# Kernel tuning notes

Measured on AMD Instinct MI355X. Metric: run time of the kernel, lower is better.

## Reference

```python
import jax, jax.numpy as jnp
import numpy as np

NUM_HEAD = 8
A_DIM = 256
M_DIM = 256
OUT_DIM = 256
KEY_DIM = A_DIM // NUM_HEAD   # 32
VALUE_DIM = M_DIM // NUM_HEAD # 32
B, NQ, NK = 128, 384, 384


def setup_inputs() -> dict:
    key = jax.random.key(0)
    ks = jax.random.split(key, 11)
    s = 0.05
    return {
        "q_data": jax.random.normal(ks[0], (B, NQ, A_DIM), jnp.float32),
        "m_data": jax.random.normal(ks[1], (B, NK, M_DIM), jnp.float32),
        "bias": jax.random.normal(ks[2], (B, NQ, NK), jnp.float32),
        "nonbatched_bias": jax.random.normal(ks[3], (NQ, NK), jnp.float32),
        "query_w": jax.random.normal(ks[4], (A_DIM, NUM_HEAD, KEY_DIM), jnp.float32) * s,
        "key_w": jax.random.normal(ks[5], (M_DIM, NUM_HEAD, KEY_DIM), jnp.float32) * s,
        "value_w": jax.random.normal(ks[6], (M_DIM, NUM_HEAD, VALUE_DIM), jnp.float32) * s,
        "gating_w": jax.random.normal(ks[7], (A_DIM, NUM_HEAD, VALUE_DIM), jnp.float32) * s,
        "gating_b": jax.random.normal(ks[8], (NUM_HEAD, VALUE_DIM), jnp.float32) * s,
        "output_w": jax.random.normal(ks[9], (NUM_HEAD, VALUE_DIM, OUT_DIM), jnp.float32) * s,
        "output_b": jax.random.normal(ks[10], (OUT_DIM,), jnp.float32) * s,
    }


def reference(q_data, m_data, bias, nonbatched_bias, query_w, key_w, value_w,
              gating_w, gating_b, output_w, output_b):
    # q: [b, q, h, c] scaled by 1/sqrt(key_dim)
    scale = KEY_DIM ** -0.5
    q = jnp.einsum('bqa,ahc->bqhc', q_data, query_w) * scale
    k = jnp.einsum('bka,ahc->bkhc', m_data, key_w)
    v = jnp.einsum('bka,ahc->bkhc', m_data, value_w)
    # logits [b, h, q, k] with per-batch bias and shared nonbatched bias
    logits = jnp.einsum('bqhc,bkhc->bhqk', q, k)
    logits = logits + bias[:, None, :, :] + nonbatched_bias[None, None, :, :]
    weights = jax.nn.softmax(logits, axis=-1)
    weighted_avg = jnp.einsum('bhqk,bkhc->bqhc', weights, v)
    # sigmoid gating
    gate = jax.nn.sigmoid(jnp.einsum('bqa,ahc->bqhc', q_data, gating_w)
                          + gating_b[None, None, :, :])
    weighted_avg = weighted_avg * gate
    # output projection
    out = jnp.einsum('bqhc,hco->bqo', weighted_avg, output_w) + output_b
    return out
```

## Files before the change

kernel.cpp:

```cpp
#include <hip/hip_runtime.h>

typedef unsigned short u16;
typedef unsigned int u32;
typedef __attribute__((ext_vector_type(8))) short bf16x8;
typedef __attribute__((ext_vector_type(4))) float f32x4;

#define BATCH 128
#define NQL   384
#define NKL   384
#define NHEAD 8
#define HD    32
#define ADIM  256
#define QSCALE 0.17677669529663689f

__device__ __forceinline__ u16 f2bf(float f) {
    union { float f; u32 u; } v; v.f = f;
    u32 r = v.u + 0x7fffu + ((v.u >> 16) & 1u);
    return (u16)(r >> 16);
}
__device__ __forceinline__ float bf2f(u16 u) {
    union { u32 u; float f; } v; v.u = ((u32)u) << 16;
    return v.f;
}
__device__ __forceinline__ u32 pk(float a, float b) {
    return (u32)f2bf(a) | ((u32)f2bf(b) << 16);
}

__global__ __launch_bounds__(256) void prep_w_kernel(
    const float* __restrict__ qw, const float* __restrict__ kw,
    const float* __restrict__ vw, const float* __restrict__ gw,
    const float* __restrict__ ow, u16* __restrict__ wt)
{
    const float* src;
    switch (blockIdx.y) {
        case 0: src = qw; break;
        case 1: src = kw; break;
        case 2: src = vw; break;
        case 3: src = gw; break;
        default: src = ow; break;
    }
    u16* dst = wt + (size_t)blockIdx.y * 65536;
    int t = threadIdx.x;
    int n0 = blockIdx.x * 16;
    for (int i = 0; i < 16; i++) {
        int n = n0 + i;
        dst[n * 256 + t] = f2bf(src[t * 256 + n]);
    }
}

__global__ __launch_bounds__(256) void proj2_kernel(
    const float* __restrict__ qd, const float* __restrict__ md,
    const u16* __restrict__ wt, const float* __restrict__ gb,
    u16* __restrict__ q_o, u16* __restrict__ k_o,
    u16* __restrict__ v_o, u16* __restrict__ g_o)
{
    const int z = blockIdx.z;
    const float* A = (z == 0) ? qd : md;
    const u16* W0 = wt + (size_t)(z == 0 ? 0 : 1) * 65536;
    const u16* W1 = wt + (size_t)(z == 0 ? 3 : 2) * 65536;
    u16* O0 = (z == 0) ? q_o : k_o;
    u16* O1 = (z == 0) ? g_o : v_o;

    const int bm = blockIdx.x * 128, bn = blockIdx.y * 128;
    const int tid = threadIdx.x;
    const int lane = tid & 63, wave = tid >> 6;
    const int col = lane & 15, quad = lane >> 4;
    const int mw = (wave & 1) * 64, nw = (wave >> 1) * 64;

    __shared__ u16 As[128][32];
    __shared__ u16 Ws0[128][32];
    __shared__ u16 Ws1[128][32];

    f32x4 acc0[4][4], acc1[4][4];
#pragma unroll
    for (int i = 0; i < 4; i++)
#pragma unroll
        for (int j = 0; j < 4; j++) {
            acc0[i][j] = (f32x4){0.f, 0.f, 0.f, 0.f};
            acc1[i][j] = (f32x4){0.f, 0.f, 0.f, 0.f};
        }

    const int arow = tid >> 1, acb = (tid & 1) * 16;
    const float* asrc = A + (size_t)(bm + arow) * 256 + acb;
    const u16*   ws0  = W0 + (size_t)(bn + arow) * 256 + acb;
    const u16*   ws1  = W1 + (size_t)(bn + arow) * 256 + acb;

    for (int k0 = 0; k0 < 256; k0 += 32) {
        __syncthreads();
        {
            float4 f0 = *(const float4*)(asrc + k0 + 0);
            float4 f1 = *(const float4*)(asrc + k0 + 4);
            float4 f2 = *(const float4*)(asrc + k0 + 8);
            float4 f3 = *(const float4*)(asrc + k0 + 12);
            uint4 u0 = make_uint4(pk(f0.x, f0.y), pk(f0.z, f0.w), pk(f1.x, f1.y), pk(f1.z, f1.w));
            uint4 u1 = make_uint4(pk(f2.x, f2.y), pk(f2.z, f2.w), pk(f3.x, f3.y), pk(f3.z, f3.w));
            *(uint4*)&As[arow][acb + 0] = u0;
            *(uint4*)&As[arow][acb + 8] = u1;
            *(uint4*)&Ws0[arow][acb + 0] = *(const uint4*)(ws0 + k0 + 0);
            *(uint4*)&Ws0[arow][acb + 8] = *(const uint4*)(ws0 + k0 + 8);
            *(uint4*)&Ws1[arow][acb + 0] = *(const uint4*)(ws1 + k0 + 0);
            *(uint4*)&Ws1[arow][acb + 8] = *(const uint4*)(ws1 + k0 + 8);
        }
        __syncthreads();
        bf16x8 bv0[4], bv1[4];
#pragma unroll
        for (int nt = 0; nt < 4; nt++) {
            bv0[nt] = *(const bf16x8*)&Ws0[nw + nt * 16 + col][quad * 8];
            bv1[nt] = *(const bf16x8*)&Ws1[nw + nt * 16 + col][quad * 8];
        }
#pragma unroll
        for (int mt = 0; mt < 4; mt++) {
            bf16x8 av = *(const bf16x8*)&As[mw + mt * 16 + col][quad * 8];
#pragma unroll
            for (int nt = 0; nt < 4; nt++) {
                acc0[mt][nt] = __builtin_amdgcn_mfma_f32_16x16x32_bf16(av, bv0[nt], acc0[mt][nt], 0, 0, 0);
                acc1[mt][nt] = __builtin_amdgcn_mfma_f32_16x16x32_bf16(av, bv1[nt], acc1[mt][nt], 0, 0, 0);
            }
        }
    }

#pragma unroll
    for (int nt = 0; nt < 4; nt++) {
        int gn = bn + nw + nt * 16 + col;
        float gbv = (z == 0) ? gb[gn] : 0.f;
#pragma unroll
        for (int mt = 0; mt < 4; mt++) {
#pragma unroll
            for (int r = 0; r < 4; r++) {
                int gm = bm + mw + mt * 16 + quad * 4 + r;
                float v0 = acc0[mt][nt][r];
                float v1 = acc1[mt][nt][r];
                if (z == 0) {
                    v0 *= QSCALE;
                    v1 = 1.f / (1.f + __expf(-(v1 + gbv)));
                }
                O0[(size_t)gm * 256 + gn] = f2bf(v0);
                O1[(size_t)gm * 256 + gn] = f2bf(v1);
            }
        }
    }
}

__global__ __launch_bounds__(256) void attn_kernel(
    const u16* __restrict__ q_ws, const u16* __restrict__ k_ws,
    const u16* __restrict__ v_ws, const u16* __restrict__ g_ws,
    const float* __restrict__ bias, const float* __restrict__ nb,
    u16* __restrict__ wa_ws)
{
    const int bi = blockIdx.x >> 3, h = blockIdx.x & 7;
    const int tid = threadIdx.x;
    const int lane = tid & 63, wave = tid >> 6;
    const int col = lane & 15, quad = lane >> 4;

    __shared__ u16 Ks[384][32];
    __shared__ u16 Vt[32 * 384];
    __shared__ __align__(16) char scratch[4][4096];
    float* Bs = (float*)scratch[wave];
    u16*   Ps = (u16*)scratch[wave];

    const u16* kg = k_ws + (size_t)bi * 384 * 256 + h * 32;
    const u16* vg = v_ws + (size_t)bi * 384 * 256 + h * 32;
    for (int f = tid * 8; f < 384 * 32; f += 256 * 8) {
        int kr = f >> 5, c = f & 31;
        *(uint4*)&Ks[kr][c] = *(const uint4*)&kg[kr * 256 + c];
    }
    for (int f = tid * 8; f < 384 * 32; f += 256 * 8) {
        int kv = f >> 5, c0 = f & 31;
        u16 tmp[8];
        *(uint4*)tmp = *(const uint4*)&vg[kv * 256 + c0];
        int kvg = kv >> 3, kvr = kv & 7;
#pragma unroll
        for (int j = 0; j < 8; j++) {
            int c = c0 + j;
            Vt[c * 384 + ((kvg ^ (c & 7)) << 3) + kvr] = tmp[j];
        }
    }
    __syncthreads();

    for (int qt = wave; qt < 24; qt += 4) {
        const int q0 = qt * 16;
        bf16x8 qf = *(const bf16x8*)(q_ws + ((size_t)(bi * 384 + q0 + col)) * 256 + h * 32 + quad * 8);

        const float* brow = bias + ((size_t)bi * 384 + q0) * 384;
        const float* nrow = nb + (size_t)q0 * 384;

        float S[24][4];
#pragma unroll
        for (int g = 0; g < 6; g++) {
#pragma unroll
            for (int i = 0; i < 4; i++) {
                int flat = lane + 64 * i;
                int row = flat >> 4, c4 = (flat & 15) << 2;
                float4 bv = *(const float4*)&brow[(size_t)row * 384 + g * 64 + c4];
                float4 nv = *(const float4*)&nrow[(size_t)row * 384 + g * 64 + c4];
                float4 sv = make_float4(bv.x + nv.x, bv.y + nv.y, bv.z + nv.z, bv.w + nv.w);
                *(float4*)&Bs[row * 64 + c4] = sv;
            }
            asm volatile("s_waitcnt lgkmcnt(0)" ::: "memory");
#pragma unroll
            for (int tt = 0; tt < 4; tt++) {
                int t = g * 4 + tt;
                f32x4 ci;
#pragma unroll
                for (int r = 0; r < 4; r++)
                    ci[r] = Bs[(quad * 4 + r) * 64 + tt * 16 + col];
                bf16x8 kf = *(const bf16x8*)&Ks[t * 16 + col][quad * 8];
                f32x4 a = __builtin_amdgcn_mfma_f32_16x16x32_bf16(qf, kf, ci, 0, 0, 0);
                S[t][0] = a[0]; S[t][1] = a[1]; S[t][2] = a[2]; S[t][3] = a[3];
            }
            asm volatile("s_waitcnt lgkmcnt(0)" ::: "memory");
        }

#pragma unroll
        for (int r = 0; r < 4; r++) {
            float m = S[0][r];
#pragma unroll
            for (int t = 1; t < 24; t++) m = fmaxf(m, S[t][r]);
#pragma unroll
            for (int o = 1; o < 16; o <<= 1) m = fmaxf(m, __shfl_xor(m, o));
            float s = 0.f;
#pragma unroll
            for (int t = 0; t < 24; t++) { float p = __expf(S[t][r] - m); S[t][r] = p; s += p; }
#pragma unroll
            for (int o = 1; o < 16; o <<= 1) s += __shfl_xor(s, o);
            float inv = 1.f / s;
#pragma unroll
            for (int t = 0; t < 24; t++) S[t][r] *= inv;
        }

        f32x4 o0 = (f32x4){0.f, 0.f, 0.f, 0.f};
        f32x4 o1 = (f32x4){0.f, 0.f, 0.f, 0.f};
#pragma unroll
        for (int g = 0; g < 6; g++) {
#pragma unroll
            for (int tt = 0; tt < 4; tt++) {
                int t = g * 4 + tt;
#pragma unroll
                for (int r = 0; r < 4; r++)
                    Ps[(quad * 4 + r) * 72 + tt * 16 + col] = f2bf(S[t][r]);
            }
            asm volatile("s_waitcnt lgkmcnt(0)" ::: "memory");
            bf16x8 a0 = *(const bf16x8*)&Ps[col * 72 + quad * 8];
            bf16x8 a1 = *(const bf16x8*)&Ps[col * 72 + 32 + quad * 8];
            const int e = col & 7;
            const int gg0 = g * 8 + quad;
            const int gg1 = gg0 + 4;
            bf16x8 b00 = *(const bf16x8*)&Vt[col * 384 + ((gg0 ^ e) << 3)];
            bf16x8 b01 = *(const bf16x8*)&Vt[col * 384 + ((gg1 ^ e) << 3)];
            bf16x8 b10 = *(const bf16x8*)&Vt[(col + 16) * 384 + ((gg0 ^ e) << 3)];
            bf16x8 b11 = *(const bf16x8*)&Vt[(col + 16) * 384 + ((gg1 ^ e) << 3)];
            o0 = __builtin_amdgcn_mfma_f32_16x16x32_bf16(a0, b00, o0, 0, 0, 0);
            o0 = __builtin_amdgcn_mfma_f32_16x16x32_bf16(a1, b01, o0, 0, 0, 0);
            o1 = __builtin_amdgcn_mfma_f32_16x16x32_bf16(a0, b10, o1, 0, 0, 0);
            o1 = __builtin_amdgcn_mfma_f32_16x16x32_bf16(a1, b11, o1, 0, 0, 0);
            asm volatile("s_waitcnt lgkmcnt(0)" ::: "memory");
        }

        const size_t rowbase = (size_t)bi * 384 + q0 + quad * 4;
#pragma unroll
        for (int r = 0; r < 4; r++) {
            size_t base = (rowbase + r) * 256 + h * 32;
            {
                size_t idx = base + col;
                wa_ws[idx] = f2bf(o0[r] * bf2f(g_ws[idx]));
            }
            {
                size_t idx = base + 16 + col;
                wa_ws[idx] = f2bf(o1[r] * bf2f(g_ws[idx]));
            }
        }
    }
}

__global__ __launch_bounds__(256) void outproj_kernel(
    const u16* __restrict__ wa, const u16* __restrict__ W,
    const float* __restrict__ ob, float* __restrict__ out)
{
    const int bm = blockIdx.x * 128, bn = blockIdx.y * 128;
    const int tid = threadIdx.x;
    const int lane = tid & 63, wave = tid >> 6;
    const int col = lane & 15, quad = lane >> 4;
    const int mw = (wave & 1) * 64, nw = (wave >> 1) * 64;

    __shared__ u16 As[128][32];
    __shared__ u16 Ws[128][32];

    f32x4 acc[4][4];
#pragma unroll
    for (int i = 0; i < 4; i++)
#pragma unroll
        for (int j = 0; j < 4; j++) acc[i][j] = (f32x4){0.f, 0.f, 0.f, 0.f};

    const int arow = tid >> 1, acb = (tid & 1) * 16;
    const u16* asrc = wa + (size_t)(bm + arow) * 256 + acb;
    const u16* wsrc = W + (size_t)(bn + arow) * 256 + acb;

    for (int k0 = 0; k0 < 256; k0 += 32) {
        __syncthreads();
        *(uint4*)&As[arow][acb + 0] = *(const uint4*)(asrc + k0 + 0);
        *(uint4*)&As[arow][acb + 8] = *(const uint4*)(asrc + k0 + 8);
        *(uint4*)&Ws[arow][acb + 0] = *(const uint4*)(wsrc + k0 + 0);
        *(uint4*)&Ws[arow][acb + 8] = *(const uint4*)(wsrc + k0 + 8);
        __syncthreads();
        bf16x8 bv[4];
#pragma unroll
        for (int nt = 0; nt < 4; nt++)
            bv[nt] = *(const bf16x8*)&Ws[nw + nt * 16 + col][quad * 8];
#pragma unroll
        for (int mt = 0; mt < 4; mt++) {
            bf16x8 av = *(const bf16x8*)&As[mw + mt * 16 + col][quad * 8];
#pragma unroll
            for (int nt = 0; nt < 4; nt++)
                acc[mt][nt] = __builtin_amdgcn_mfma_f32_16x16x32_bf16(av, bv[nt], acc[mt][nt], 0, 0, 0);
        }
    }

#pragma unroll
    for (int nt = 0; nt < 4; nt++) {
        int gn = bn + nw + nt * 16 + col;
        float obv = ob[gn];
#pragma unroll
        for (int mt = 0; mt < 4; mt++) {
#pragma unroll
            for (int r = 0; r < 4; r++) {
                int gm = bm + mw + mt * 16 + quad * 4 + r;
                out[(size_t)gm * 256 + gn] = acc[mt][nt][r] + obv;
            }
        }
    }
}

extern "C" void kernel_launch(void* const* d_in, const int* in_sizes, int n_in,
                              void* d_out, int out_size, void* d_ws, size_t ws_size,
                              hipStream_t stream)
{
    const float* q_data = (const float*)d_in[0];
    const float* m_data = (const float*)d_in[1];
    const float* bias   = (const float*)d_in[2];
    const float* nb     = (const float*)d_in[3];
    const float* qw     = (const float*)d_in[4];
    const float* kw     = (const float*)d_in[5];
    const float* vw     = (const float*)d_in[6];
    const float* gw     = (const float*)d_in[7];
    const float* gb     = (const float*)d_in[8];
    const float* ow     = (const float*)d_in[9];
    const float* ob     = (const float*)d_in[10];
    float* out = (float*)d_out;

    char* ws = (char*)d_ws;
    u16* wt = (u16*)ws;
    const size_t PROJ = (size_t)BATCH * NQL * 256;
    u16* q_ws  = (u16*)(ws + (1 << 20));
    u16* k_ws  = q_ws + PROJ;
    u16* v_ws  = k_ws + PROJ;
    u16* g_ws  = v_ws + PROJ;
    u16* wa_ws = g_ws + PROJ;

    prep_w_kernel<<<dim3(16, 5), 256, 0, stream>>>(qw, kw, vw, gw, ow, wt);
    proj2_kernel<<<dim3(384, 2, 2), 256, 0, stream>>>(q_data, m_data, wt, gb,
                                                      q_ws, k_ws, v_ws, g_ws);
    attn_kernel<<<dim3(1024), 256, 0, stream>>>(q_ws, k_ws, v_ws, g_ws,
                                                bias, nb, wa_ws);
    outproj_kernel<<<dim3(384, 2), 256, 0, stream>>>(wa_ws, wt + 4 * 65536, ob, out);
}
```

Before: 445.5 us.

## Pre-swizzle combined bias to bf16 fragments and widen projection GEMM tiles with async LDS loads

A new prep kernel sums the batched and non-batched bias once and stores it as bf16 in MFMA accumulator-fragment order. The attention kernel then loads each bias fragment directly as the MFMA C input, instead of every head re-reading and adding two fp32 bias tensors through LDS. The projection and output GEMMs move to one 256-wide N tile per block, with weight (and activation) tiles loaded into LDS through global_load_lds, and launch bounds set to allow two blocks per CU. The attention output buffer now reuses the q buffer, and block order is changed to head-major. Storing the bias in bf16 reduces precision, and the head-major ordering may reduce L2 reuse of K/V and bias across heads.

```diff
diff --git a/kernel.cpp b/kernel.cpp
--- a/kernel.cpp
+++ b/kernel.cpp
@@ -2,6 +2,7 @@
 
 typedef unsigned short u16;
 typedef unsigned int u32;
+typedef unsigned long long u64;
 typedef __attribute__((ext_vector_type(8))) short bf16x8;
 typedef __attribute__((ext_vector_type(4))) float f32x4;
 
@@ -25,6 +26,12 @@
 __device__ __forceinline__ u32 pk(float a, float b) {
     return (u32)f2bf(a) | ((u32)f2bf(b) << 16);
 }
+__device__ __forceinline__ void async_cp16(const void* g, void* l) {
+    __builtin_amdgcn_global_load_lds(
+        (const __attribute__((address_space(1))) u32*)g,
+        (__attribute__((address_space(3))) u32*)(u32)(u64)l,
+        16, 0, 0);
+}
 
 __global__ __launch_bounds__(256) void prep_w_kernel(
     const float* __restrict__ qw, const float* __restrict__ kw,
@@ -48,45 +55,70 @@
     }
 }
 
-__global__ __launch_bounds__(256) void proj2_kernel(
+__global__ __launch_bounds__(256) void prep_bias_kernel(
+    const float* __restrict__ bias, const float* __restrict__ nb,
+    u16* __restrict__ bias_sw)
+{
+    const int qt = blockIdx.x, b = blockIdx.y;
+    const int t = threadIdx.x;
+    const int lane = t & 63, sub = t >> 6;
+    const int col = lane & 15, quad = lane >> 4;
+    const float* bb = bias + ((size_t)b * 384 + qt * 16) * 384;
+    const float* nn = nb + (size_t)qt * 16 * 384;
+    u16* outb = bias_sw + ((size_t)b * 24 + qt) * 24 * 256;
+#pragma unroll
+    for (int i = 0; i < 6; i++) {
+        int kt = sub + i * 4;
+        int c = kt * 16 + col;
+        u16 v[4];
+#pragma unroll
+        for (int r = 0; r < 4; r++) {
+            int q = quad * 4 + r;
+            v[r] = f2bf(bb[(size_t)q * 384 + c] + nn[(size_t)q * 384 + c]);
+        }
+        *(uint2*)&outb[(size_t)kt * 256 + lane * 4] = *(uint2*)v;
+    }
+}
+
+__global__ __launch_bounds__(256, 2) void proj_kernel(
     const float* __restrict__ qd, const float* __restrict__ md,
     const u16* __restrict__ wt, const float* __restrict__ gb,
     u16* __restrict__ q_o, u16* __restrict__ k_o,
     u16* __restrict__ v_o, u16* __restrict__ g_o)
 {
-    const int z = blockIdx.z;
-    const float* A = (z == 0) ? qd : md;
-    const u16* W0 = wt + (size_t)(z == 0 ? 0 : 1) * 65536;
-    const u16* W1 = wt + (size_t)(z == 0 ? 3 : 2) * 65536;
-    u16* O0 = (z == 0) ? q_o : k_o;
-    u16* O1 = (z == 0) ? g_o : v_o;
-
-    const int bm = blockIdx.x * 128, bn = blockIdx.y * 128;
+    const int widx = blockIdx.x;
+    const int bm = blockIdx.y * 128;
+    const int side = blockIdx.z;
+    const float* A = side ? md : qd;
+    const int wsel = side ? (widx ? 2 : 1) : (widx ? 3 : 0);
+    const u16* W = wt + (size_t)wsel * 65536;
+    u16* O = side ? (widx ? v_o : k_o) : (widx ? g_o : q_o);
+    const int mode = side ? 0 : (widx ? 2 : 1);
+
     const int tid = threadIdx.x;
     const int lane = tid & 63, wave = tid >> 6;
     const int col = lane & 15, quad = lane >> 4;
-    const int mw = (wave & 1) * 64, nw = (wave >> 1) * 64;
-
-    __shared__ u16 As[128][32];
-    __shared__ u16 Ws0[128][32];
-    __shared__ u16 Ws1[128][32];
-
-    f32x4 acc0[4][4], acc1[4][4];
+    const int mw = (wave & 1) * 64, nsl = (wave >> 1) * 128;
+
+    __shared__ u16 Abf[128][32];
+    __shared__ u16 Wb[256][32];
+
+    f32x4 acc[4][8];
 #pragma unroll
     for (int i = 0; i < 4; i++)
 #pragma unroll
-        for (int j = 0; j < 4; j++) {
-            acc0[i][j] = (f32x4){0.f, 0.f, 0.f, 0.f};
-            acc1[i][j] = (f32x4){0.f, 0.f, 0.f, 0.f};
-        }
+        for (int j = 0; j < 8; j++) acc[i][j] = (f32x4){0.f, 0.f, 0.f, 0.f};
 
     const int arow = tid >> 1, acb = (tid & 1) * 16;
     const float* asrc = A + (size_t)(bm + arow) * 256 + acb;
-    const u16*   ws0  = W0 + (size_t)(bn + arow) * 256 + acb;
-    const u16*   ws1  = W1 + (size_t)(bn + arow) * 256 + acb;
+    const int wrow = tid >> 2, wcb = (tid & 3) * 8;
 
     for (int k0 = 0; k0 < 256; k0 += 32) {
         __syncthreads();
+#pragma unroll
+        for (int i = 0; i < 4; i++)
+            async_cp16(W + (size_t)(i * 64 + wrow) * 256 + k0 + wcb,
+                       (char*)Wb + i * 4096 + tid * 16);
         {
             float4 f0 = *(const float4*)(asrc + k0 + 0);
             float4 f1 = *(const float4*)(asrc + k0 + 4);
@@ -94,48 +126,39 @@
             float4 f3 = *(const float4*)(asrc + k0 + 12);
             uint4 u0 = make_uint4(pk(f0.x, f0.y), pk(f0.z, f0.w), pk(f1.x, f1.y), pk(f1.z, f1.w));
             uint4 u1 = make_uint4(pk(f2.x, f2.y), pk(f2.z, f2.w), pk(f3.x, f3.y), pk(f3.z, f3.w));
-            *(uint4*)&As[arow][acb + 0] = u0;
-            *(uint4*)&As[arow][acb + 8] = u1;
-            *(uint4*)&Ws0[arow][acb + 0] = *(const uint4*)(ws0 + k0 + 0);
-            *(uint4*)&Ws0[arow][acb + 8] = *(const uint4*)(ws0 + k0 + 8);
-            *(uint4*)&Ws1[arow][acb + 0] = *(const uint4*)(ws1 + k0 + 0);
-            *(uint4*)&Ws1[arow][acb + 8] = *(const uint4*)(ws1 + k0 + 8);
-        }
+            *(uint4*)&Abf[arow][acb + 0] = u0;
+            *(uint4*)&Abf[arow][acb + 8] = u1;
+        }
+        asm volatile("s_waitcnt vmcnt(0)" ::: "memory");
         __syncthreads();
-        bf16x8 bv0[4], bv1[4];
-#pragma unroll
-        for (int nt = 0; nt < 4; nt++) {
-            bv0[nt] = *(const bf16x8*)&Ws0[nw + nt * 16 + col][quad * 8];
-            bv1[nt] = *(const bf16x8*)&Ws1[nw + nt * 16 + col][quad * 8];
-        }
-#pragma unroll
-        for (int mt = 0; mt < 4; mt++) {
-            bf16x8 av = *(const bf16x8*)&As[mw + mt * 16 + col][quad * 8];
-#pragma unroll
-            for (int nt = 0; nt < 4; nt++) {
-                acc0[mt][nt] = __builtin_amdgcn_mfma_f32_16x16x32_bf16(av, bv0[nt], acc0[mt][nt], 0, 0, 0);
-                acc1[mt][nt] = __builtin_amdgcn_mfma_f32_16x16x32_bf16(av, bv1[nt], acc1[mt][nt], 0, 0, 0);
-            }
-        }
-    }
-
-#pragma unroll
-    for (int nt = 0; nt < 4; nt++) {
-        int gn = bn + nw + nt * 16 + col;
-        float gbv = (z == 0) ? gb[gn] : 0.f;
+
+        bf16x8 av[4], bv[8];
+#pragma unroll
+        for (int mt = 0; mt < 4; mt++)
+            av[mt] = *(const bf16x8*)&Abf[mw + mt * 16 + col][quad * 8];
+#pragma unroll
+        for (int j = 0; j < 8; j++)
+            bv[j] = *(const bf16x8*)&Wb[nsl + j * 16 + col][quad * 8];
+#pragma unroll
+        for (int mt = 0; mt < 4; mt++)
+#pragma unroll
+            for (int j = 0; j < 8; j++)
+                acc[mt][j] = __builtin_amdgcn_mfma_f32_16x16x32_bf16(av[mt], bv[j], acc[mt][j], 0, 0, 0);
+    }
+
+#pragma unroll
+    for (int j = 0; j < 8; j++) {
+        int gn = nsl + j * 16 + col;
+        float gbv = (mode == 2) ? gb[gn] : 0.f;
 #pragma unroll
         for (int mt = 0; mt < 4; mt++) {
 #pragma unroll
             for (int r = 0; r < 4; r++) {
                 int gm = bm + mw + mt * 16 + quad * 4 + r;
-                float v0 = acc0[mt][nt][r];
-                float v1 = acc1[mt][nt][r];
-                if (z == 0) {
-                    v0 *= QSCALE;
-                    v1 = 1.f / (1.f + __expf(-(v1 + gbv)));
-                }
-                O0[(size_t)gm * 256 + gn] = f2bf(v0);
-                O1[(size_t)gm * 256 + gn] = f2bf(v1);
+                float v = acc[mt][j][r];
+                if (mode == 1) v *= QSCALE;
+                if (mode == 2) v = 1.f / (1.f + __expf(-(v + gbv)));
+                O[(size_t)gm * 256 + gn] = f2bf(v);
             }
         }
     }
@@ -144,19 +167,16 @@
 __global__ __launch_bounds__(256) void attn_kernel(
     const u16* __restrict__ q_ws, const u16* __restrict__ k_ws,
     const u16* __restrict__ v_ws, const u16* __restrict__ g_ws,
-    const float* __restrict__ bias, const float* __restrict__ nb,
-    u16* __restrict__ wa_ws)
-{
-    const int bi = blockIdx.x >> 3, h = blockIdx.x & 7;
+    const u16* __restrict__ bias_sw, u16* __restrict__ wa_ws)
+{
+    const int h = blockIdx.x >> 7, bi = blockIdx.x & 127;
     const int tid = threadIdx.x;
     const int lane = tid & 63, wave = tid >> 6;
     const int col = lane & 15, quad = lane >> 4;
 
     __shared__ u16 Ks[384][32];
     __shared__ u16 Vt[32 * 384];
-    __shared__ __align__(16) char scratch[4][4096];
-    float* Bs = (float*)scratch[wave];
-    u16*   Ps = (u16*)scratch[wave];
+    __shared__ u16 Ps[4][16][72];
 
     const u16* kg = k_ws + (size_t)bi * 384 * 256 + h * 32;
     const u16* vg = v_ws + (size_t)bi * 384 * 256 + h * 32;
@@ -180,68 +200,53 @@
     for (int qt = wave; qt < 24; qt += 4) {
         const int q0 = qt * 16;
         bf16x8 qf = *(const bf16x8*)(q_ws + ((size_t)(bi * 384 + q0 + col)) * 256 + h * 32 + quad * 8);
-
-        const float* brow = bias + ((size_t)bi * 384 + q0) * 384;
-        const float* nrow = nb + (size_t)q0 * 384;
+        const u16* bfr = bias_sw + ((size_t)(bi * 24 + qt)) * 24 * 256 + lane * 4;
 
         float S[24][4];
 #pragma unroll
+        for (int t = 0; t < 24; t++) {
+            uint2 bw = *(const uint2*)(bfr + (size_t)t * 256);
+            f32x4 ci;
+            ci[0] = bf2f((u16)(bw.x & 0xffff));
+            ci[1] = bf2f((u16)(bw.x >> 16));
+            ci[2] = bf2f((u16)(bw.y & 0xffff));
+            ci[3] = bf2f((u16)(bw.y >> 16));
+            bf16x8 kf = *(const bf16x8*)&Ks[t * 16 + col][quad * 8];
+            f32x4 a = __builtin_amdgcn_mfma_f32_16x16x32_bf16(qf, kf, ci, 0, 0, 0);
+            S[t][0] = a[0]; S[t][1] = a[1]; S[t][2] = a[2]; S[t][3] = a[3];
+        }
+
+#pragma unroll
+        for (int r = 0; r < 4; r++) {
+            float m = S[0][r];
+#pragma unroll
+            for (int t = 1; t < 24; t++) m = fmaxf(m, S[t][r]);
+#pragma unroll
+            for (int o = 1; o < 16; o <<= 1) m = fmaxf(m, __shfl_xor(m, o));
+            float s = 0.f;
+#pragma unroll
+            for (int t = 0; t < 24; t++) { float p = __expf(S[t][r] - m); S[t][r] = p; s += p; }
+#pragma unroll
+            for (int o = 1; o < 16; o <<= 1) s += __shfl_xor(s, o);
+            float inv = 1.f / s;
+#pragma unroll
+            for (int t = 0; t < 24; t++) S[t][r] *= inv;
+        }
+
+        f32x4 o0 = (f32x4){0.f, 0.f, 0.f, 0.f};
+        f32x4 o1 = (f32x4){0.f, 0.f, 0.f, 0.f};
+#pragma unroll
         for (int g = 0; g < 6; g++) {
-#pragma unroll
-            for (int i = 0; i < 4; i++) {
-                int flat = lane + 64 * i;
-                int row = flat >> 4, c4 = (flat & 15) << 2;
-                float4 bv = *(const float4*)&brow[(size_t)row * 384 + g * 64 + c4];
-                float4 nv = *(const float4*)&nrow[(size_t)row * 384 + g * 64 + c4];
-                float4 sv = make_float4(bv.x + nv.x, bv.y + nv.y, bv.z + nv.z, bv.w + nv.w);
-                *(float4*)&Bs[row * 64 + c4] = sv;
-            }
-            asm volatile("s_waitcnt lgkmcnt(0)" ::: "memory");
 #pragma unroll
             for (int tt = 0; tt < 4; tt++) {
                 int t = g * 4 + tt;
-                f32x4 ci;
 #pragma unroll
                 for (int r = 0; r < 4; r++)
-                    ci[r] = Bs[(quad * 4 + r) * 64 + tt * 16 + col];
-                bf16x8 kf = *(const bf16x8*)&Ks[t * 16 + col][quad * 8];
-                f32x4 a = __builtin_amdgcn_mfma_f32_16x16x32_bf16(qf, kf, ci, 0, 0, 0);
-                S[t][0] = a[0]; S[t][1] = a[1]; S[t][2] = a[2]; S[t][3] = a[3];
+                    Ps[wave][quad * 4 + r][tt * 16 + col] = f2bf(S[t][r]);
             }
             asm volatile("s_waitcnt lgkmcnt(0)" ::: "memory");
-        }
-
-#pragma unroll
-        for (int r = 0; r < 4; r++) {
-            float m = S[0][r];
-#pragma unroll
-            for (int t = 1; t < 24; t++) m = fmaxf(m, S[t][r]);
-#pragma unroll
-            for (int o = 1; o < 16; o <<= 1) m = fmaxf(m, __shfl_xor(m, o));
-            float s = 0.f;
-#pragma unroll
-            for (int t = 0; t < 24; t++) { float p = __expf(S[t][r] - m); S[t][r] = p; s += p; }
-#pragma unroll
-            for (int o = 1; o < 16; o <<= 1) s += __shfl_xor(s, o);
-            float inv = 1.f / s;
-#pragma unroll
-            for (int t = 0; t < 24; t++) S[t][r] *= inv;
-        }
-
-        f32x4 o0 = (f32x4){0.f, 0.f, 0.f, 0.f};
-        f32x4 o1 = (f32x4){0.f, 0.f, 0.f, 0.f};
-#pragma unroll
-        for (int g = 0; g < 6; g++) {
-#pragma unroll
-            for (int tt = 0; tt < 4; tt++) {
-                int t = g * 4 + tt;
-#pragma unroll
-                for (int r = 0; r < 4; r++)
-                    Ps[(quad * 4 + r) * 72 + tt * 16 + col] = f2bf(S[t][r]);
-            }
-            asm volatile("s_waitcnt lgkmcnt(0)" ::: "memory");
-            bf16x8 a0 = *(const bf16x8*)&Ps[col * 72 + quad * 8];
-            bf16x8 a1 = *(const bf16x8*)&Ps[col * 72 + 32 + quad * 8];
+            bf16x8 a0 = *(const bf16x8*)&Ps[wave][col][quad * 8];
+            bf16x8 a1 = *(const bf16x8*)&Ps[wave][col][32 + quad * 8];
             const int e = col & 7;
             const int gg0 = g * 8 + quad;
             const int gg1 = gg0 + 4;
@@ -272,59 +277,64 @@
     }
 }
 
-__global__ __launch_bounds__(256) void outproj_kernel(
+__global__ __launch_bounds__(256, 2) void outproj_kernel(
     const u16* __restrict__ wa, const u16* __restrict__ W,
     const float* __restrict__ ob, float* __restrict__ out)
 {
-    const int bm = blockIdx.x * 128, bn = blockIdx.y * 128;
+    const int bm = blockIdx.x * 128;
     const int tid = threadIdx.x;
     const int lane = tid & 63, wave = tid >> 6;
     const int col = lane & 15, quad = lane >> 4;
-    const int mw = (wave & 1) * 64, nw = (wave >> 1) * 64;
-
-    __shared__ u16 As[128][32];
-    __shared__ u16 Ws[128][32];
-
-    f32x4 acc[4][4];
+    const int mw = (wave & 1) * 64, nsl = (wave >> 1) * 128;
+
+    __shared__ u16 Abf[128][32];
+    __shared__ u16 Wb[256][32];
+
+    f32x4 acc[4][8];
 #pragma unroll
     for (int i = 0; i < 4; i++)
 #pragma unroll
-        for (int j = 0; j < 4; j++) acc[i][j] = (f32x4){0.f, 0.f, 0.f, 0.f};
-
-    const int arow = tid >> 1, acb = (tid & 1) * 16;
-    const u16* asrc = wa + (size_t)(bm + arow) * 256 + acb;
-    const u16* wsrc = W + (size_t)(bn + arow) * 256 + acb;
+        for (int j = 0; j < 8; j++) acc[i][j] = (f32x4){0.f, 0.f, 0.f, 0.f};
+
+    const int wrow = tid >> 2, wcb = (tid & 3) * 8;
 
     for (int k0 = 0; k0 < 256; k0 += 32) {
         __syncthreads();
-        *(uint4*)&As[arow][acb + 0] = *(const uint4*)(asrc + k0 + 0);
-        *(uint4*)&As[arow][acb + 8] = *(const uint4*)(asrc + k0 + 8);
-        *(uint4*)&Ws[arow][acb + 0] = *(const uint4*)(wsrc + k0 + 0);
-        *(uint4*)&Ws[arow][acb + 8] = *(const uint4*)(wsrc + k0 + 8);
+#pragma unroll
+        for (int i = 0; i < 2; i++)
+            async_cp16(wa + (size_t)(bm + i * 64 + wrow) * 256 + k0 + wcb,
+                       (char*)Abf + i * 4096 + tid * 16);
+#pragma unroll
+        for (int i = 0; i < 4; i++)
+            async_cp16(W + (size_t)(i * 64 + wrow) * 256 + k0 + wcb,
+                       (char*)Wb + i * 4096 + tid * 16);
+        asm volatile("s_waitcnt vmcnt(0)" ::: "memory");
         __syncthreads();
-        bf16x8 bv[4];
-#pragma unroll
-        for (int nt = 0; nt < 4; nt++)
-            bv[nt] = *(const bf16x8*)&Ws[nw + nt * 16 + col][quad * 8];
-#pragma unroll
-        for (int mt = 0; mt < 4; mt++) {
-            bf16x8 av = *(const bf16x8*)&As[mw + mt * 16 + col][quad * 8];
-#pragma unroll
-            for (int nt = 0; nt < 4; nt++)
-                acc[mt][nt] = __builtin_amdgcn_mfma_f32_16x16x32_bf16(av, bv[nt], acc[mt][nt], 0, 0, 0);
-        }
-    }
-
-#pragma unroll
-    for (int nt = 0; nt < 4; nt++) {
-        int gn = bn + nw + nt * 16 + col;
+
+        bf16x8 av[4], bv[8];
+#pragma unroll
+        for (int mt = 0; mt < 4; mt++)
+            av[mt] = *(const bf16x8*)&Abf[mw + mt * 16 + col][quad * 8];
+#pragma unroll
+        for (int j = 0; j < 8; j++)
+            bv[j] = *(const bf16x8*)&Wb[nsl + j * 16 + col][quad * 8];
+#pragma unroll
+        for (int mt = 0; mt < 4; mt++)
+#pragma unroll
+            for (int j = 0; j < 8; j++)
+                acc[mt][j] = __builtin_amdgcn_mfma_f32_16x16x32_bf16(av[mt], bv[j], acc[mt][j], 0, 0, 0);
+    }
+
+#pragma unroll
+    for (int j = 0; j < 8; j++) {
+        int gn = nsl + j * 16 + col;
         float obv = ob[gn];
 #pragma unroll
         for (int mt = 0; mt < 4; mt++) {
 #pragma unroll
             for (int r = 0; r < 4; r++) {
                 int gm = bm + mw + mt * 16 + quad * 4 + r;
-                out[(size_t)gm * 256 + gn] = acc[mt][nt][r] + obv;
+                out[(size_t)gm * 256 + gn] = acc[mt][j][r] + obv;
             }
         }
     }
@@ -354,12 +364,14 @@
     u16* k_ws  = q_ws + PROJ;
     u16* v_ws  = k_ws + PROJ;
     u16* g_ws  = v_ws + PROJ;
-    u16* wa_ws = g_ws + PROJ;
+    u16* bias_sw = g_ws + PROJ;
+    u16* wa_ws = q_ws;
 
     prep_w_kernel<<<dim3(16, 5), 256, 0, stream>>>(qw, kw, vw, gw, ow, wt);
-    proj2_kernel<<<dim3(384, 2, 2), 256, 0, stream>>>(q_data, m_data, wt, gb,
-                                                      q_ws, k_ws, v_ws, g_ws);
+    prep_bias_kernel<<<dim3(24, 128), 256, 0, stream>>>(bias, nb, bias_sw);
+    proj_kernel<<<dim3(2, 384, 2), 256, 0, stream>>>(q_data, m_data, wt, gb,
+                                                     q_ws, k_ws, v_ws, g_ws);
     attn_kernel<<<dim3(1024), 256, 0, stream>>>(q_ws, k_ws, v_ws, g_ws,
-                                                bias, nb, wa_ws);
-    outproj_kernel<<<dim3(384, 2), 256, 0, stream>>>(wa_ws, wt + 4 * 65536, ob, out);
-}
+                                                bias_sw, wa_ws);
+    outproj_kernel<<<dim3(384), 256, 0, stream>>>(wa_ws, wt + 4 * 65536, ob, out);
+}
```

Result: slower. 462.5 us (+3.8%).
